# Performance work log

Hardware: AMD Instinct MI355X
Metric: run time of the kernel (lower is better)

The kernel has to match this reference:

```python
import jax, jax.numpy as jnp
import numpy as np
from jax import lax

V, E, W, L, T, H, B = 10000, 256, 256, 512, 64, 512, 64  # vocab, emb, weight, seq_len, answer_len, hidden, batch


def _lstm_cell(x, h, c, Wih, Whh, bih, bhh):
    # PyTorch gate order: i, f, g, o
    g = x @ Wih.T + bih + h @ Whh.T + bhh
    i, f, gg, o = jnp.split(g, 4, axis=-1)
    c = jax.nn.sigmoid(f) * c + jax.nn.sigmoid(i) * jnp.tanh(gg)
    h = jax.nn.sigmoid(o) * jnp.tanh(c)
    return h, c


def setup_inputs() -> dict:
    key = jax.random.key(0)
    ks = jax.random.split(key, 18)
    s = 1.0 / np.sqrt(H)
    p = lambda k, shape, sc: (jax.random.normal(k, shape, jnp.float32) * sc)
    return {
        "input_ids": jax.random.randint(ks[0], (B, L), 0, V),
        "emb_W": p(ks[1], (V, E), 0.05),
        "enc_Wih": p(ks[2], (4 * H, E), s), "enc_Whh": p(ks[3], (4 * H, H), s),
        "enc_bih": p(ks[4], (4 * H,), s), "enc_bhh": p(ks[5], (4 * H,), s),
        "dec_Wih": p(ks[6], (4 * H, E), s), "dec_Whh": p(ks[7], (4 * H, H), s),
        "dec_bih": p(ks[8], (4 * H,), s), "dec_bhh": p(ks[9], (4 * H,), s),
        "W1_w": p(ks[10], (W, H), s), "W1_b": p(ks[11], (W,), s),
        "W2_w": p(ks[12], (W, H), s), "W2_b": p(ks[13], (W,), s),
        "vt_w": p(ks[14], (1, W), s), "vt_b": p(ks[15], (1,), s),
        "h0": jax.random.normal(ks[16], (B, H), jnp.float32),
    }


def reference(input_ids, emb_W, enc_Wih, enc_Whh, enc_bih, enc_bhh,
              dec_Wih, dec_Whh, dec_bih, dec_bhh,
              W1_w, W1_b, W2_w, W2_b, vt_w, vt_b, h0):
    x = emb_W[input_ids]                      # [B, L, E]
    xs = jnp.swapaxes(x, 0, 1)                # [L, B, E]

    def enc_step(carry, xt):
        h, c = carry
        h, c = _lstm_cell(xt, h, c, enc_Wih, enc_Whh, enc_bih, enc_bhh)
        return (h, c), h

    zeros = jnp.zeros((B, H), x.dtype)
    _, enc_states = lax.scan(enc_step, (zeros, zeros), xs)   # [L, B, H]

    c0 = enc_states[-1]                       # cell init = last encoder output (as in source)
    blend1 = enc_states @ W1_w.T + W1_b       # [L, B, W] -- same every step, hoisted
    x_dec = jnp.zeros((B, E), x.dtype)        # decoder_input stays zeros in the original

    def dec_step(carry, _):
        h, c = carry
        h, c = _lstm_cell(x_dec, h, c, dec_Wih, dec_Whh, dec_bih, dec_bhh)
        blend = jnp.tanh(blend1 + h @ W2_w.T + W2_b)          # [L, B, W]
        scores = (blend @ vt_w.T)[..., 0] + vt_b[0]           # [L, B]
        logp = jax.nn.log_softmax(scores, axis=0)             # softmax over L (per batch col)
        return (h, c), logp

    _, probs = lax.scan(dec_step, (h0, c0), None, length=T)   # [T, L, B]
    return jnp.transpose(probs, (1, 2, 0))                    # [L, B, T] (stack dim=2)
```

## Files before the change

### kernel.cpp

```cpp
#include <hip/hip_runtime.h>

#define NB 64
#define NL 512
#define NT 64
#define NH 512
#define NE 256
#define NW 256
#define NBNH (NB * NH)
#define RS 16

typedef __attribute__((ext_vector_type(8))) short bf16x8;
typedef __attribute__((ext_vector_type(4))) float f32x4;
typedef unsigned short u16;
typedef unsigned int u32;
typedef unsigned long long u64;

#define STM 0x4000400040004000ull
#define CLRM 0xBFFFBFFFBFFFBFFFull

__device__ __forceinline__ float bf2f(u16 v){
  union { u32 u; float f; } x; x.u = ((u32)v) << 16; return x.f;
}
__device__ __forceinline__ u16 f2bf(float f){
  union { float f; u32 u; } x; x.f = f;
  return (u16)((x.u + 0x7FFFu + ((x.u >> 16) & 1u)) >> 16);
}
__device__ __forceinline__ float sigm(float x){ return 1.f / (1.f + __expf(-x)); }
__device__ __forceinline__ float tanh_(float x){ float e = __expf(2.f * x); return 1.f - 2.f / (e + 1.f); }

__device__ __forceinline__ u64 ald64(const u64* p){
  return __hip_atomic_load(p, __ATOMIC_RELAXED, __HIP_MEMORY_SCOPE_AGENT);
}
__device__ __forceinline__ u32 ald32(const u32* p){
  return __hip_atomic_load(p, __ATOMIC_RELAXED, __HIP_MEMORY_SCOPE_AGENT);
}
__device__ __forceinline__ void ast64(u64* p, u64 v){
  __hip_atomic_store(p, v, __ATOMIC_RELAXED, __HIP_MEMORY_SCOPE_AGENT);
}
__device__ __forceinline__ void ast32(u32* p, u32 v){
  __hip_atomic_store(p, v, __ATOMIC_RELAXED, __HIP_MEMORY_SCOPE_AGENT);
}
__device__ __forceinline__ void st64(u64* p, u64 v){
  __hip_atomic_store(p, v, __ATOMIC_RELAXED, __HIP_MEMORY_SCOPE_WORKGROUP);
}
__device__ __forceinline__ void st32(u32* p, u32 v){
  __hip_atomic_store(p, v, __ATOMIC_RELAXED, __HIP_MEMORY_SCOPE_WORKGROUP);
}
__device__ __forceinline__ bf16x8 mk8(u64 a, u64 b){
  union { u64 q[2]; bf16x8 v; } u; u.q[0] = a; u.q[1] = b; return u.v;
}
__device__ __forceinline__ u32 xcc_id(){
  u32 x;
  asm volatile("s_getreg_b32 %0, hwreg(HW_REG_XCC_ID)" : "=s"(x));
  return x & 7u;
}
__device__ __forceinline__ void burn32(f32x4* bacc, bf16x8 junk){
#pragma unroll
  for(int i = 0; i < 8; ++i)
#pragma unroll
    for(int g = 0; g < 4; ++g)
      bacc[g] = __builtin_amdgcn_mfma_f32_16x16x32_bf16(junk, junk, bacc[g], 0, 0, 0);
}
__device__ __forceinline__ void burn_sink(f32x4* bacc){
  asm volatile("" :: "v"(bacc[0][0]), "v"(bacc[1][0]), "v"(bacc[2][0]), "v"(bacc[3][0]));
}

__global__ void fill_kernel(u32* p, u32 v){
  p[blockIdx.x * 256 + threadIdx.x] = v;
}

__global__ void cvt_kernel(const float* __restrict__ src, u16* __restrict__ dst, int n){
  const int i = blockIdx.x * 256 + threadIdx.x;
  if(i < n) dst[i] = f2bf(src[i]);
}

__global__ void __launch_bounds__(256, 1) enc_kernel(
    const int* __restrict__ ids, const u16* __restrict__ emb,
    const u16* __restrict__ Wih, const u16* __restrict__ Whh,
    const float* __restrict__ bih, const float* __restrict__ bhh,
    const u16* __restrict__ W1,  const float* __restrict__ b1,
    u16* hroll, u16* bl, u32* cnt, u32* flags)
{
  extern __shared__ char dynsm[];
  f32x4* pacc = (f32x4*)dynsm;
  __shared__ u32 srank;

  const int lane = threadIdx.x & 63;
  const int wvl  = threadIdx.x >> 6;
  const int col  = lane & 15;
  const int quad = lane >> 4;

  const u32 xcd = xcc_id();
  if(xcd >= 4){
    f32x4 bacc[4];
#pragma unroll
    for(int g = 0; g < 4; ++g) bacc[g] = (f32x4){0.f, 0.f, 0.f, 0.f};
    const bf16x8 junk = {0, 0, 0, 0, 0, 0, 0, 0};
    const u32* dp = cnt + 64 + (xcd & 3);
    for(;;){
      if(ald32(dp) != 0u) break;
      burn32(bacc, junk); burn32(bacc, junk);
      burn32(bacc, junk); burn32(bacc, junk);
    }
    burn_sink(bacc);
    return;
  }
  if(threadIdx.x == 0) srank = atomicAdd(&cnt[xcd], 1u);
  __syncthreads();
  const u32 rank = srank;
  const int btile = (int)xcd;
  u32* fbase = flags + (size_t)xcd * (RS * 32);

  if(rank >= 16){
    if(rank >= 32) return;
    f32x4 bacc[4];
#pragma unroll
    for(int g = 0; g < 4; ++g) bacc[g] = (f32x4){0.f, 0.f, 0.f, 0.f};
    const bf16x8 junk = {0, 0, 0, 0, 0, 0, 0, 0};
    if(wvl != 0){
      const u32* dp = cnt + 64 + xcd;
      for(;;){
        if(ald32(dp) != 0u) break;
        burn32(bacc, junk); burn32(bacc, junk);
        burn32(bacc, junk); burn32(bacc, junk);
      }
      burn_sink(bacc);
      return;
    }
    const int n1 = ((int)rank - 16) * 16 + col;
    bf16x8 w1f[16];
    const u16* w1p = W1 + (size_t)n1 * NH + quad * 8;
#pragma unroll
    for(int i = 0; i < 16; ++i) w1f[i] = *(const bf16x8*)(w1p + 32 * i);
    const float b1f = b1[n1];
    const int arow = btile * 16 + col;

    for(int t = 0; t < NL; ++t){
      const int slot = t & (RS - 1);
      const u32 fwant = (u32)((t >> 4) & 1);
      {
        const u32* fp = fbase + slot * 32;
        for(;;){
          const u32 f = ald32(fp + (lane & 31));
          if(__ballot(f == fwant) == ~0ull) break;
          burn32(bacc, junk);
        }
      }
      const u16* ha = hroll + (size_t)slot * NBNH + (size_t)arow * NH + quad * 8;
      const u64 want = fwant ? STM : 0ull;
      u64 hw[32];
      for(;;){
        bool ok = true;
#pragma unroll
        for(int i = 0; i < 16; ++i){
          const u64* p = (const u64*)(ha + 32 * i);
          hw[2 * i]     = ald64(p);
          hw[2 * i + 1] = ald64(p + 1);
          ok = ok && ((hw[2 * i] & STM) == want) && ((hw[2 * i + 1] & STM) == want);
        }
        if(__ballot(ok) == ~0ull) break;
      }
      f32x4 a2 = {0.f, 0.f, 0.f, 0.f};
#pragma unroll
      for(int i = 0; i < 16; ++i)
        a2 = __builtin_amdgcn_mfma_f32_16x16x32_bf16(
               mk8(hw[2 * i] & CLRM, hw[2 * i + 1] & CLRM), w1f[i], a2, 0, 0, 0);
#pragma unroll
      for(int r = 0; r < 4; ++r){
        const int b = btile * 16 + quad * 4 + r;
        bl[((size_t)t * NB + b) * NW + n1] = f2bf(a2[r] + b1f);
      }
    }
    burn_sink(bacc);
    return;
  }

  const int mtile  = (int)rank * 2 + (wvl >> 1);
  const int khalf  = wvl & 1;
  const int pairid = wvl >> 1;
  const bool lowerw = (khalf == 0);
  const int j  = mtile * 16 + col;
  const int ab = btile * 16 + col;

  float bias[4];
  const u16* wx[4];
  bf16x8 whr[8][4];
#pragma unroll
  for(int g = 0; g < 4; ++g){
    const int row = g * NH + j;
    bias[g] = bih[row] + bhh[row];
    wx[g] = Wih + (size_t)row * NE + khalf * 128 + quad * 8;
    const u16* whp = Whh + (size_t)row * NH + khalf * 256 + quad * 8;
#pragma unroll
    for(int i = 0; i < 8; ++i)
      whr[i][g] = *(const bf16x8*)(whp + 32 * i);
  }
  const int* idp = ids + ab * NL;
  float creg[4] = {0.f, 0.f, 0.f, 0.f};

  u64 hb[16];
  f32x4 acc[4];

  {
    const u16* xr = emb + (size_t)idp[0] * NE + khalf * 128 + quad * 8;
#pragma unroll
    for(int g = 0; g < 4; ++g) acc[g] = (f32x4){0.f, 0.f, 0.f, 0.f};
#pragma unroll
    for(int k0 = 0; k0 < 128; k0 += 32){
      const bf16x8 af = *(const bf16x8*)(xr + k0);
#pragma unroll
      for(int g = 0; g < 4; ++g)
        acc[g] = __builtin_amdgcn_mfma_f32_16x16x32_bf16(af, *(const bf16x8*)(wx[g] + k0), acc[g], 0, 0, 0);
    }
  }

  for(int t = 0; t < NL; ++t){
    if(t > 0){
#pragma unroll
      for(int i = 0; i < 8; ++i){
        const bf16x8 af = mk8(hb[2 * i], hb[2 * i + 1]);
#pragma unroll
        for(int g = 0; g < 4; ++g)
          acc[g] = __builtin_amdgcn_mfma_f32_16x16x32_bf16(af, whr[i][g], acc[g], 0, 0, 0);
      }
    }
    bf16x8 xa0, xa1, xa2, xa3;
    const u16* xr = (t + 1 < NL) ? (emb + (size_t)idp[t + 1] * NE + khalf * 128 + quad * 8) : emb;
    xa0 = *(const bf16x8*)(xr);
    xa1 = *(const bf16x8*)(xr + 32);
    xa2 = *(const bf16x8*)(xr + 64);
    xa3 = *(const bf16x8*)(xr + 96);

    const int slot = t & (RS - 1);
    const u32 fphase = (u32)((t >> 4) & 1);

    if(!lowerw){
#pragma unroll
      for(int g = 0; g < 4; ++g)
        pacc[(((t & 1) * 2 + pairid) * 4 + g) * 64 + lane] = acc[g];
    }
    __syncthreads();
    if(lowerw){
#pragma unroll
      for(int g = 0; g < 4; ++g){
        const f32x4 pa = pacc[(((t & 1) * 2 + pairid) * 4 + g) * 64 + lane];
        acc[g][0] += pa[0]; acc[g][1] += pa[1]; acc[g][2] += pa[2]; acc[g][3] += pa[3];
      }
      const u64 pst = fphase ? STM : 0ull;
      u16* ho = hroll + (size_t)slot * NBNH;
#pragma unroll
      for(int r = 0; r < 4; ++r){
        const float gi = acc[0][r] + bias[0];
        const float gf = acc[1][r] + bias[1];
        const float gg = acc[2][r] + bias[2];
        const float go = acc[3][r] + bias[3];
        creg[r] = sigm(gf) * creg[r] + sigm(gi) * tanh_(gg);
        const u32 raw  = (u32)f2bf(sigm(go) * tanh_(creg[r]));
        const u32 pair = raw | (((u32)__shfl_xor((int)raw, 1, 64)) << 16);
        const u32 hi   = (u32)__shfl_xor((int)pair, 2, 64);
        if((col & 3) == 0){
          const int row = btile * 16 + quad * 4 + r;
          st64((u64*)(ho + (size_t)row * NH + mtile * 16 + col),
               ((u64)pair | ((u64)hi << 32)) | pst);
        }
      }
      if(lane == 0) st32(fbase + slot * 32 + mtile, fphase);
    }
    if(t + 1 < NL){
#pragma unroll
      for(int g = 0; g < 4; ++g) acc[g] = (f32x4){0.f, 0.f, 0.f, 0.f};
#pragma unroll
      for(int g = 0; g < 4; ++g){
        acc[g] = __builtin_amdgcn_mfma_f32_16x16x32_bf16(xa0, *(const bf16x8*)(wx[g]),      acc[g], 0, 0, 0);
        acc[g] = __builtin_amdgcn_mfma_f32_16x16x32_bf16(xa1, *(const bf16x8*)(wx[g] + 32), acc[g], 0, 0, 0);
        acc[g] = __builtin_amdgcn_mfma_f32_16x16x32_bf16(xa2, *(const bf16x8*)(wx[g] + 64), acc[g], 0, 0, 0);
        acc[g] = __builtin_amdgcn_mfma_f32_16x16x32_bf16(xa3, *(const bf16x8*)(wx[g] + 96), acc[g], 0, 0, 0);
      }
      {
        const u32* fp = fbase + slot * 32 + khalf * 16;
        for(;;){
          const u32 f = ald32(fp + (lane & 15));
          if(__ballot(f == fphase) == ~0ull) break;
        }
      }
      {
        const u16* ha = hroll + (size_t)slot * NBNH + (size_t)ab * NH + khalf * 256 + quad * 8;
        const u64 want = fphase ? STM : 0ull;
        for(;;){
          bool ok = true;
#pragma unroll
          for(int i = 0; i < 8; ++i){
            const u64* p = (const u64*)(ha + 32 * i);
            hb[2 * i]     = ald64(p);
            hb[2 * i + 1] = ald64(p + 1);
            ok = ok && ((hb[2 * i] & STM) == want) && ((hb[2 * i + 1] & STM) == want);
          }
          if(__ballot(ok) == ~0ull) break;
        }
#pragma unroll
        for(int i = 0; i < 16; ++i) hb[i] &= CLRM;
      }
    }
  }
  if(rank == 0 && threadIdx.x == 0) ast32(cnt + 64 + (u32)xcd, 1u);
}

__global__ void __launch_bounds__(256, 1) dec_kernel(
    const u16* __restrict__ Whh, const float* __restrict__ bih, const float* __restrict__ bhh,
    const float* __restrict__ W2, const float* __restrict__ b2,
    const float* __restrict__ vt, const float* __restrict__ vtb,
    const u16* __restrict__ bl,  u16* hroll,
    const float* __restrict__ h0f,
    u16* hdX, float* __restrict__ out, u32* cnt, u32* flags)
{
  extern __shared__ char dynsm[];
  f32x4* pacc = (f32x4*)dynsm;
  __shared__ u32 srank;
  __shared__ __align__(16) float h_f[NH];
  __shared__ __align__(16) float u_lds[NW];
  __shared__ __align__(16) float vt_lds[NW];
  __shared__ float red[8];

  const int tid  = threadIdx.x;
  const int lane = tid & 63;
  const int wvl  = tid >> 6;
  const int col  = lane & 15;
  const int quad = lane >> 4;

  const u32 xcd = xcc_id();
  if(xcd < 4){
    if(tid == 0) srank = atomicAdd(&cnt[8 + xcd], 1u);
    __syncthreads();
    const u32 rank = srank;
    const int btile = (int)xcd;
    u32* fbase = flags + (size_t)xcd * (RS * 32);

    if(rank >= 16){
      if(rank >= 32 || tid >= 128) return;
      const int jm = (int)rank - 16;
      const int row = btile * 16 + (tid & 15);
      const int chunk = jm * 8 + ((tid >> 4) & 7);
      const int fmt = chunk >> 2;
      f32x4 bacc[4];
#pragma unroll
      for(int g = 0; g < 4; ++g) bacc[g] = (f32x4){0.f, 0.f, 0.f, 0.f};
      const bf16x8 junk = {0, 0, 0, 0, 0, 0, 0, 0};
      for(int t = 0; t < NT; ++t){
        const int slot = t & (RS - 1);
        const u32 fwant = (u32)((t >> 4) & 1);
        for(;;){
          if(ald32(fbase + slot * 32 + fmt) == fwant) break;
          burn32(bacc, junk);
        }
        const u64* rp = (const u64*)(hroll + (size_t)slot * NBNH) + (size_t)row * (NH / 4) + chunk;
        const u64 want = fwant ? STM : 0ull;
        u64 v;
        for(;;){
          v = ald64(rp);
          if((v & STM) == want) break;
        }
        ast64((u64*)(hdX + (size_t)t * NBNH) + (size_t)row * (NH / 4) + chunk,
              (v & CLRM) | STM);
      }
      burn_sink(bacc);
      return;
    }

    const int mtile  = (int)rank * 2 + (wvl >> 1);
    const int khalf  = wvl & 1;
    const int pairid = wvl >> 1;
    const bool lowerw = (khalf == 0);
    const int j  = mtile * 16 + col;
    const int ab = btile * 16 + col;

    float bias[4];
    bf16x8 whr[8][4];
#pragma unroll
    for(int g = 0; g < 4; ++g){
      const int row = g * NH + j;
      bias[g] = bih[row] + bhh[row];
      const u16* whp = Whh + (size_t)row * NH + khalf * 256 + quad * 8;
#pragma unroll
      for(int i = 0; i < 8; ++i)
        whr[i][g] = *(const bf16x8*)(whp + 32 * i);
    }
    float creg[4] = {0.f, 0.f, 0.f, 0.f};
    if(lowerw){
#pragma unroll
      for(int r = 0; r < 4; ++r){
        const int ci = (btile * 16 + quad * 4 + r) * NH + j;
        creg[r] = bf2f((u16)(hroll[(size_t)15 * NBNH + ci] & 0xBFFFu));
      }
    }
    u64 hb[16];
    f32x4 acc[4];

    {
      const float* hp = h0f + (size_t)ab * NH + khalf * 256 + quad * 8;
#pragma unroll
      for(int g = 0; g < 4; ++g) acc[g] = (f32x4){0.f, 0.f, 0.f, 0.f};
#pragma unroll
      for(int i = 0; i < 8; ++i){
        const f32x4 a0 = *(const f32x4*)(hp + 32 * i);
        const f32x4 a1 = *(const f32x4*)(hp + 32 * i + 4);
        bf16x8 af;
#pragma unroll
        for(int q = 0; q < 4; ++q){ af[q] = (short)f2bf(a0[q]); af[q + 4] = (short)f2bf(a1[q]); }
#pragma unroll
        for(int g = 0; g < 4; ++g)
          acc[g] = __builtin_amdgcn_mfma_f32_16x16x32_bf16(af, whr[i][g], acc[g], 0, 0, 0);
      }
    }

    for(int t = 0; t < NT; ++t){
      if(t > 0){
#pragma unroll
        for(int g = 0; g < 4; ++g) acc[g] = (f32x4){0.f, 0.f, 0.f, 0.f};
#pragma unroll
        for(int i = 0; i < 8; ++i){
          const bf16x8 af = mk8(hb[2 * i], hb[2 * i + 1]);
#pragma unroll
          for(int g = 0; g < 4; ++g)
            acc[g] = __builtin_amdgcn_mfma_f32_16x16x32_bf16(af, whr[i][g], acc[g], 0, 0, 0);
        }
      }
      const int slot = t & (RS - 1);
      const u32 fphase = (u32)((t >> 4) & 1);
      if(!lowerw){
#pragma unroll
        for(int g = 0; g < 4; ++g)
          pacc[(((t & 1) * 2 + pairid) * 4 + g) * 64 + lane] = acc[g];
      }
      __syncthreads();
      if(lowerw){
#pragma unroll
        for(int g = 0; g < 4; ++g){
          const f32x4 pa = pacc[(((t & 1) * 2 + pairid) * 4 + g) * 64 + lane];
          acc[g][0] += pa[0]; acc[g][1] += pa[1]; acc[g][2] += pa[2]; acc[g][3] += pa[3];
        }
        const u64 pst = fphase ? STM : 0ull;
        u16* ho = hroll + (size_t)slot * NBNH;
#pragma unroll
        for(int r = 0; r < 4; ++r){
          const float gi = acc[0][r] + bias[0];
          const float gf = acc[1][r] + bias[1];
          const float gg = acc[2][r] + bias[2];
          const float go = acc[3][r] + bias[3];
          creg[r] = sigm(gf) * creg[r] + sigm(gi) * tanh_(gg);
          const u32 raw  = (u32)f2bf(sigm(go) * tanh_(creg[r]));
          const u32 pair = raw | (((u32)__shfl_xor((int)raw, 1, 64)) << 16);
          const u32 hi   = (u32)__shfl_xor((int)pair, 2, 64);
          if((col & 3) == 0){
            const int row = btile * 16 + quad * 4 + r;
            st64((u64*)(ho + (size_t)row * NH + mtile * 16 + col),
                 ((u64)pair | ((u64)hi << 32)) | pst);
          }
        }
        if(lane == 0) st32(fbase + slot * 32 + mtile, fphase);
      }
      if(t + 1 < NT){
        {
          const u32* fp = fbase + slot * 32 + khalf * 16;
          for(;;){
            const u32 f = ald32(fp + (lane & 15));
            if(__ballot(f == fphase) == ~0ull) break;
          }
        }
        const u16* ha = hroll + (size_t)slot * NBNH + (size_t)ab * NH + khalf * 256 + quad * 8;
        const u64 want = fphase ? STM : 0ull;
        for(;;){
          bool ok = true;
#pragma unroll
          for(int i = 0; i < 8; ++i){
            const u64* p = (const u64*)(ha + 32 * i);
            hb[2 * i]     = ald64(p);
            hb[2 * i + 1] = ald64(p + 1);
            ok = ok && ((hb[2 * i] & STM) == want) && ((hb[2 * i + 1] & STM) == want);
          }
          if(__ballot(ok) == ~0ull) break;
        }
#pragma unroll
        for(int i = 0; i < 16; ++i) hb[i] &= CLRM;
      }
    }
    return;
  }

  if(tid == 0) srank = atomicAdd(&cnt[12], 1u);
  __syncthreads();
  const int wid = (int)srank;

  vt_lds[tid] = vt[tid];
  const float vtbf = vtb[0];
  __syncthreads();

  f32x4 bacc[4];
#pragma unroll
  for(int g = 0; g < 4; ++g) bacc[g] = (f32x4){0.f, 0.f, 0.f, 0.f};
  const bf16x8 junk = {0, 0, 0, 0, 0, 0, 0, 0};

  for(int tk = wid; tk < NT * NB; tk += 128){
    const int t = tk >> 6;
    const int b = tk & 63;

    {
      const u32* hp = (const u32*)(hdX + (size_t)t * NBNH + (size_t)b * NH);
      u32 v;
      for(;;){
        v = ald32(hp + tid);
        burn32(bacc, junk);
        const int ok = ((v & 0x40004000u) == 0x40004000u) ? 1 : 0;
        if(__syncthreads_and(ok)) break;
      }
      h_f[2 * tid]     = bf2f((u16)(v & 0xBFFFu));
      h_f[2 * tid + 1] = bf2f((u16)((v >> 16) & 0xBFFFu));
    }
    __syncthreads();

    {
      const float* w2r = W2 + (size_t)tid * NH;
      float s = b2[tid];
#pragma unroll 4
      for(int k = 0; k < NH; k += 4){
        const f32x4 hv = *(const f32x4*)(&h_f[k]);
        const f32x4 wv = *(const f32x4*)(w2r + k);
        s += hv[0] * wv[0] + hv[1] * wv[1] + hv[2] * wv[2] + hv[3] * wv[3];
      }
      u_lds[tid] = s;
    }
    __syncthreads();

    float a0, a1;
#pragma unroll
    for(int e = 0; e < 2; ++e){
      const int l = tid + e * 256;
      const u16* br = bl + (size_t)(l * NB + b) * NW;
      float p = 0.f;
#pragma unroll 2
      for(int w0 = 0; w0 < NW; w0 += 8){
        const bf16x8 bv = *(const bf16x8*)(br + w0);
#pragma unroll
        for(int q = 0; q < 8; ++q)
          p += vt_lds[w0 + q] * tanh_(bf2f((u16)bv[q]) + u_lds[w0 + q]);
      }
      if(e == 0) a0 = p + vtbf; else a1 = p + vtbf;
    }

    float mx = fmaxf(a0, a1);
#pragma unroll
    for(int off = 32; off > 0; off >>= 1) mx = fmaxf(mx, __shfl_xor(mx, off, 64));
    if(lane == 0) red[wvl] = mx;
    __syncthreads();
    mx = fmaxf(fmaxf(red[0], red[1]), fmaxf(red[2], red[3]));
    float es = __expf(a0 - mx) + __expf(a1 - mx);
#pragma unroll
    for(int off = 32; off > 0; off >>= 1) es += __shfl_xor(es, off, 64);
    if(lane == 0) red[4 + wvl] = es;
    __syncthreads();
    const float lse = mx + logf(red[4] + red[5] + red[6] + red[7]);
    out[((size_t)tid * NB + b) * NT + t]         = a0 - lse;
    out[((size_t)(tid + 256) * NB + b) * NT + t] = a1 - lse;
    __syncthreads();
  }
  burn_sink(bacc);
}

extern "C" void kernel_launch(void* const* d_in, const int* in_sizes, int n_in,
                              void* d_out, int out_size, void* d_ws, size_t ws_size,
                              hipStream_t stream)
{
  (void)in_sizes; (void)n_in; (void)out_size; (void)ws_size;
  const int*   ids  = (const int*)d_in[0];
  const float* emb  = (const float*)d_in[1];
  const float* eWih = (const float*)d_in[2];
  const float* eWhh = (const float*)d_in[3];
  const float* ebih = (const float*)d_in[4];
  const float* ebhh = (const float*)d_in[5];
  const float* dWhh = (const float*)d_in[7];
  const float* dbih = (const float*)d_in[8];
  const float* dbhh = (const float*)d_in[9];
  const float* W1   = (const float*)d_in[10];
  const float* b1   = (const float*)d_in[11];
  const float* W2   = (const float*)d_in[12];
  const float* b2   = (const float*)d_in[13];
  const float* vt   = (const float*)d_in[14];
  const float* vtb  = (const float*)d_in[15];
  const float* h0   = (const float*)d_in[16];

  char* ws = (char*)d_ws;
  u16* bl     = (u16*)ws; ws += (size_t)NL * NB * NW * 2;
  u16* hroll  = (u16*)ws; ws += (size_t)RS * NBNH * 2;
  u16* X      = (u16*)ws; ws += (size_t)10000 * NE * 2;
  u16* eWih_b = (u16*)ws; ws += (size_t)4 * NH * NE * 2;
  u16* eWhh_b = (u16*)ws; ws += (size_t)4 * NH * NH * 2;
  u16* dWhh_b = (u16*)ws; ws += (size_t)4 * NH * NH * 2;
  u16* W1_b   = (u16*)ws; ws += (size_t)NW * NH * 2;
  u32* cnt    = (u32*)ws; ws += 1024;
  u32* flags  = (u32*)ws; ws += (size_t)4 * RS * 32 * 4;

  hipLaunchKernelGGL(fill_kernel, dim3((RS * NBNH / 2) / 256), dim3(256), 0, stream,
                     (u32*)hroll, 0x40004000u);
  hipLaunchKernelGGL(fill_kernel, dim3(8), dim3(256), 0, stream, flags, 1u);
  hipLaunchKernelGGL(fill_kernel, dim3(1), dim3(256), 0, stream, cnt, 0u);
  hipLaunchKernelGGL(cvt_kernel, dim3(10000), dim3(256), 0, stream, emb,  X,      10000 * NE);
  hipLaunchKernelGGL(cvt_kernel, dim3(2048),  dim3(256), 0, stream, eWih, eWih_b, 4 * NH * NE);
  hipLaunchKernelGGL(cvt_kernel, dim3(4096),  dim3(256), 0, stream, eWhh, eWhh_b, 4 * NH * NH);
  hipLaunchKernelGGL(cvt_kernel, dim3(4096),  dim3(256), 0, stream, dWhh, dWhh_b, 4 * NH * NH);
  hipLaunchKernelGGL(cvt_kernel, dim3(512),   dim3(256), 0, stream, W1,   W1_b,   NW * NH);

  hipLaunchKernelGGL(enc_kernel, dim3(256), dim3(256), 92160, stream,
                     ids, X, eWih_b, eWhh_b, ebih, ebhh, W1_b, b1, hroll, bl, cnt, flags);
  hipLaunchKernelGGL(dec_kernel, dim3(256), dim3(256), 92160, stream,
                     dWhh_b, dbih, dbhh, W2, b2, vt, vtb, bl, hroll, h0, X,
                     (float*)d_out, cnt, flags);
}
```

Baseline: 3.987 ms.

## Drop XCD-local rolling buffer and flags in decoder; publish h directly to hdX

The decoder recurrence blocks no longer rank themselves per XCD or exchange hidden state through a rolling buffer plus per-tile flags and copy-forwarder blocks. Each step writes h, tagged with a ready bit, straight into the per-step hdX buffer with agent-scope atomics, and both the recurrence readers and the attention blocks poll those tags. Block roles now come from blockIdx, which frees 128 more blocks for attention (stride 192 instead of 128). The encoder also gains a vmcnt drain before setting each flag. In exchange, cross-XCD traffic may make the recurrence handoff slower, and correctness depends on the tag bits in hdX starting out clear and on all 64 recurrence blocks being co-resident.

```diff
diff --git a/kernel.cpp b/kernel.cpp
--- a/kernel.cpp
+++ b/kernel.cpp
@@ -45,6 +45,9 @@
 }
 __device__ __forceinline__ void st32(u32* p, u32 v){
   __hip_atomic_store(p, v, __ATOMIC_RELAXED, __HIP_MEMORY_SCOPE_WORKGROUP);
+}
+__device__ __forceinline__ void vm_drain(){
+  asm volatile("s_waitcnt vmcnt(0)" ::: "memory");
 }
 __device__ __forceinline__ bf16x8 mk8(u64 a, u64 b){
   union { u64 q[2]; bf16x8 v; } u; u.q[0] = a; u.q[1] = b; return u.v;
@@ -264,6 +267,7 @@
                ((u64)pair | ((u64)hi << 32)) | pst);
         }
       }
+      vm_drain();
       if(lane == 0) st32(fbase + slot * 32 + mtile, fphase);
     }
     if(t + 1 < NL){
@@ -309,13 +313,12 @@
     const u16* __restrict__ Whh, const float* __restrict__ bih, const float* __restrict__ bhh,
     const float* __restrict__ W2, const float* __restrict__ b2,
     const float* __restrict__ vt, const float* __restrict__ vtb,
-    const u16* __restrict__ bl,  u16* hroll,
+    const u16* __restrict__ bl,  const u16* __restrict__ hroll,
     const float* __restrict__ h0f,
-    u16* hdX, float* __restrict__ out, u32* cnt, u32* flags)
+    u16* hdX, float* __restrict__ out)
 {
   extern __shared__ char dynsm[];
   f32x4* pacc = (f32x4*)dynsm;
-  __shared__ u32 srank;
   __shared__ __align__(16) float h_f[NH];
   __shared__ __align__(16) float u_lds[NW];
   __shared__ __align__(16) float vt_lds[NW];
@@ -327,46 +330,10 @@
   const int col  = lane & 15;
   const int quad = lane >> 4;
 
-  const u32 xcd = xcc_id();
-  if(xcd < 4){
-    if(tid == 0) srank = atomicAdd(&cnt[8 + xcd], 1u);
-    __syncthreads();
-    const u32 rank = srank;
-    const int btile = (int)xcd;
-    u32* fbase = flags + (size_t)xcd * (RS * 32);
-
-    if(rank >= 16){
-      if(rank >= 32 || tid >= 128) return;
-      const int jm = (int)rank - 16;
-      const int row = btile * 16 + (tid & 15);
-      const int chunk = jm * 8 + ((tid >> 4) & 7);
-      const int fmt = chunk >> 2;
-      f32x4 bacc[4];
-#pragma unroll
-      for(int g = 0; g < 4; ++g) bacc[g] = (f32x4){0.f, 0.f, 0.f, 0.f};
-      const bf16x8 junk = {0, 0, 0, 0, 0, 0, 0, 0};
-      for(int t = 0; t < NT; ++t){
-        const int slot = t & (RS - 1);
-        const u32 fwant = (u32)((t >> 4) & 1);
-        for(;;){
-          if(ald32(fbase + slot * 32 + fmt) == fwant) break;
-          burn32(bacc, junk);
-        }
-        const u64* rp = (const u64*)(hroll + (size_t)slot * NBNH) + (size_t)row * (NH / 4) + chunk;
-        const u64 want = fwant ? STM : 0ull;
-        u64 v;
-        for(;;){
-          v = ald64(rp);
-          if((v & STM) == want) break;
-        }
-        ast64((u64*)(hdX + (size_t)t * NBNH) + (size_t)row * (NH / 4) + chunk,
-              (v & CLRM) | STM);
-      }
-      burn_sink(bacc);
-      return;
-    }
-
-    const int mtile  = (int)rank * 2 + (wvl >> 1);
+  if(blockIdx.x < 64){
+    const int btile  = (int)blockIdx.x >> 4;
+    const int rank   = (int)blockIdx.x & 15;
+    const int mtile  = rank * 2 + (wvl >> 1);
     const int khalf  = wvl & 1;
     const int pairid = wvl >> 1;
     const bool lowerw = (khalf == 0);
@@ -424,8 +391,6 @@
             acc[g] = __builtin_amdgcn_mfma_f32_16x16x32_bf16(af, whr[i][g], acc[g], 0, 0, 0);
         }
       }
-      const int slot = t & (RS - 1);
-      const u32 fphase = (u32)((t >> 4) & 1);
       if(!lowerw){
 #pragma unroll
         for(int g = 0; g < 4; ++g)
@@ -438,8 +403,7 @@
           const f32x4 pa = pacc[(((t & 1) * 2 + pairid) * 4 + g) * 64 + lane];
           acc[g][0] += pa[0]; acc[g][1] += pa[1]; acc[g][2] += pa[2]; acc[g][3] += pa[3];
         }
-        const u64 pst = fphase ? STM : 0ull;
-        u16* ho = hroll + (size_t)slot * NBNH;
+        u16* hn = hdX + (size_t)t * NBNH;
 #pragma unroll
         for(int r = 0; r < 4; ++r){
           const float gi = acc[0][r] + bias[0];
@@ -447,27 +411,18 @@
           const float gg = acc[2][r] + bias[2];
           const float go = acc[3][r] + bias[3];
           creg[r] = sigm(gf) * creg[r] + sigm(gi) * tanh_(gg);
-          const u32 raw  = (u32)f2bf(sigm(go) * tanh_(creg[r]));
-          const u32 pair = raw | (((u32)__shfl_xor((int)raw, 1, 64)) << 16);
+          const u32 stv  = (u32)f2bf(sigm(go) * tanh_(creg[r])) | 0x4000u;
+          const u32 pair = stv | (((u32)__shfl_xor((int)stv, 1, 64)) << 16);
           const u32 hi   = (u32)__shfl_xor((int)pair, 2, 64);
           if((col & 3) == 0){
             const int row = btile * 16 + quad * 4 + r;
-            st64((u64*)(ho + (size_t)row * NH + mtile * 16 + col),
-                 ((u64)pair | ((u64)hi << 32)) | pst);
+            ast64((u64*)(hn + (size_t)row * NH + mtile * 16 + col),
+                  (u64)pair | ((u64)hi << 32));
           }
         }
-        if(lane == 0) st32(fbase + slot * 32 + mtile, fphase);
       }
       if(t + 1 < NT){
-        {
-          const u32* fp = fbase + slot * 32 + khalf * 16;
-          for(;;){
-            const u32 f = ald32(fp + (lane & 15));
-            if(__ballot(f == fphase) == ~0ull) break;
-          }
-        }
-        const u16* ha = hroll + (size_t)slot * NBNH + (size_t)ab * NH + khalf * 256 + quad * 8;
-        const u64 want = fphase ? STM : 0ull;
+        const u16* ha = hdX + (size_t)t * NBNH + (size_t)ab * NH + khalf * 256 + quad * 8;
         for(;;){
           bool ok = true;
 #pragma unroll
@@ -475,7 +430,7 @@
             const u64* p = (const u64*)(ha + 32 * i);
             hb[2 * i]     = ald64(p);
             hb[2 * i + 1] = ald64(p + 1);
-            ok = ok && ((hb[2 * i] & STM) == want) && ((hb[2 * i + 1] & STM) == want);
+            ok = ok && ((hb[2 * i] & STM) == STM) && ((hb[2 * i + 1] & STM) == STM);
           }
           if(__ballot(ok) == ~0ull) break;
         }
@@ -486,9 +441,7 @@
     return;
   }
 
-  if(tid == 0) srank = atomicAdd(&cnt[12], 1u);
-  __syncthreads();
-  const int wid = (int)srank;
+  const int wid = (int)blockIdx.x - 64;
 
   vt_lds[tid] = vt[tid];
   const float vtbf = vtb[0];
@@ -499,7 +452,7 @@
   for(int g = 0; g < 4; ++g) bacc[g] = (f32x4){0.f, 0.f, 0.f, 0.f};
   const bf16x8 junk = {0, 0, 0, 0, 0, 0, 0, 0};
 
-  for(int tk = wid; tk < NT * NB; tk += 128){
+  for(int tk = wid; tk < NT * NB; tk += 192){
     const int t = tk >> 6;
     const int b = tk & 63;
 
@@ -612,5 +565,5 @@
                      ids, X, eWih_b, eWhh_b, ebih, ebhh, W1_b, b1, hroll, bl, cnt, flags);
   hipLaunchKernelGGL(dec_kernel, dim3(256), dim3(256), 92160, stream,
                      dWhh_b, dbih, dbhh, W2, b2, vt, vtb, bl, hroll, h0, X,
-                     (float*)d_out, cnt, flags);
-}
+                     (float*)d_out);
+}
```

Result: faster. 3.542 ms (-11.2%).
